# Performance work log

Measured on AMD Instinct MI355X. Metric: run time of the kernel, lower is better.

The kernel has to match this reference:

```python
import jax, jax.numpy as jnp
import numpy as np

B, T, K = 8, 512, 8
V_WORD, V_BIWORD, V_GAZ = 100000, 200000, 300000
D_WORD, D_BIWORD, D_GAZ = 50, 50, 50
HIDDEN = 256
H = HIDDEN // 2          # per-direction lattice LSTM hidden
D_IN = D_WORD + D_BIWORD # use_bigram=True
N_LABELS = 20


def setup_inputs() -> dict:
    key = jax.random.key(0)
    ks = jax.random.split(key, 16)
    word_inputs = jax.random.randint(ks[0], (B, T), 0, V_WORD)
    biword_inputs = jax.random.randint(ks[1], (B, T), 0, V_BIWORD)
    gaz_word_ids = jax.random.randint(ks[2], (B, T, K), 0, V_GAZ)
    lengths = jax.random.randint(ks[3], (B, T, K), 2, 10)  # lexicon word length in [2,9]
    pos = jnp.arange(T)[None, :, None]
    starts = pos - lengths + 1  # state index of the word's start position
    present = jax.random.bernoulli(ks[4], 0.4, (B, T, K))
    gaz_mask = present & (starts >= 0)
    gaz_starts = jnp.clip(starts, 0)
    mask = jnp.ones((B, T), dtype=jnp.int32)

    def u(k, shape, fan):
        s = 1.0 / np.sqrt(fan)
        return jax.random.uniform(k, shape, jnp.float32, -s, s)

    return dict(
        word_inputs=word_inputs, biword_inputs=biword_inputs,
        gaz_word_ids=gaz_word_ids, gaz_starts=gaz_starts,
        gaz_mask=gaz_mask, mask=mask,
        word_table=u(ks[5], (V_WORD, D_WORD), D_WORD),
        biword_table=u(ks[6], (V_BIWORD, D_BIWORD), D_BIWORD),
        gaz_table=u(ks[7], (V_GAZ, D_GAZ), D_GAZ),
        W_ih=u(ks[8], (3 * H, D_IN), D_IN),
        W_hh=u(ks[9], (3 * H, H), H),
        b_lstm=jnp.zeros((3 * H,), jnp.float32),
        Wa_ih=u(ks[10], (H, D_IN), D_IN),
        Wa_hh=u(ks[11], (H, H), H),
        b_alpha=jnp.zeros((H,), jnp.float32),
        Ww_ih=u(ks[12], (3 * H, D_GAZ), D_GAZ),
        Ww_hh=u(ks[13], (3 * H, H), H),
        b_word=jnp.zeros((3 * H,), jnp.float32),
        W_tag=u(ks[14], (N_LABELS, HIDDEN), HIDDEN),
        b_tag=jnp.zeros((N_LABELS,), jnp.float32),
    )


def lattice_lstm(x, gaz_emb, gaz_starts, gaz_mask,
                 W_ih, W_hh, b_lstm, Wa_ih, Wa_hh, b_alpha, Ww_ih, Ww_hh, b_word):
    Bn, Tn, _ = x.shape
    Hh = W_hh.shape[1]
    h0 = jnp.zeros((Bn, Hh), x.dtype)
    c0 = jnp.zeros((Bn, Hh), x.dtype)
    hist0 = jnp.zeros((Bn, Tn, Hh), x.dtype)
    xs = (jnp.arange(Tn), x.transpose(1, 0, 2), gaz_emb.transpose(1, 0, 2, 3),
          gaz_starts.transpose(1, 0, 2), gaz_mask.transpose(1, 0, 2))

    def step(carry, inp):
        h_prev, c_prev, h_hist, c_hist = carry
        j, x_j, ge_j, s_j, m_j = inp
        # gather (h, c) at the word start positions  [B,K,H]
        h_s = jnp.take_along_axis(h_hist, s_j[..., None], axis=1)
        c_s = jnp.take_along_axis(c_hist, s_j[..., None], axis=1)
        # WordLSTMCell: word memory cells for edges ending at j
        wg = (jnp.einsum('bkd,gd->bkg', ge_j, Ww_ih)
              + jnp.einsum('bkh,gh->bkg', h_s, Ww_hh) + b_word)
        i_w, f_w, g_w = jnp.split(wg, 3, axis=-1)
        c_w = jax.nn.sigmoid(f_w) * c_s + jax.nn.sigmoid(i_w) * jnp.tanh(g_w)
        # MultiInputLSTMCell char gates (i, o, g)
        g3 = x_j @ W_ih.T + h_prev @ W_hh.T + b_lstm
        i, o, g = jnp.split(g3, 3, axis=-1)
        i, o, g = jax.nn.sigmoid(i), jax.nn.sigmoid(o), jnp.tanh(g)
        # gated aggregation over word cells: alpha = exp(sigmoid(.)), softmax with exp(i)
        alpha = jax.nn.sigmoid((x_j @ Wa_ih.T)[:, None, :]
                               + jnp.einsum('bkh,gh->bkg', c_w, Wa_hh) + b_alpha)
        mk = m_j[..., None].astype(x_j.dtype)  # [B,K,1]
        w_word = mk * jnp.exp(alpha)
        w_char = jnp.exp(i)
        c_soft = (w_char * g + (w_word * c_w).sum(1)) / (w_char + w_word.sum(1))
        c_cpl = (1.0 - i) * c_prev + i * g  # coupled path when no word edges
        has_word = m_j.any(axis=1)[:, None]
        c_new = jnp.where(has_word, c_soft, c_cpl)
        h_new = o * jnp.tanh(c_new)
        return (h_new, c_new, h_hist.at[:, j].set(h_new), c_hist.at[:, j].set(c_new)), h_new

    _, hs = jax.lax.scan(step, (h0, c0, hist0, hist0), xs)
    return hs.transpose(1, 0, 2)  # [B,T,H]


def reference(word_inputs, biword_inputs, gaz_word_ids, gaz_starts, gaz_mask, mask,
              word_table, biword_table, gaz_table, W_ih, W_hh, b_lstm,
              Wa_ih, Wa_hh, b_alpha, Ww_ih, Ww_hh, b_word, W_tag, b_tag):
    # embedding + bigram concat (dropout is identity in eval)
    x = jnp.concatenate([word_table[word_inputs], biword_table[biword_inputs]], axis=-1)
    gaz_emb = gaz_table[gaz_word_ids]  # [B,T,K,Dg]
    fwd = lattice_lstm(x, gaz_emb, gaz_starts, gaz_mask,
                       W_ih, W_hh, b_lstm, Wa_ih, Wa_hh, b_alpha, Ww_ih, Ww_hh, b_word)
    # source bug: the 'backward' pass also calls self.forward_lstm -> identical output
    lstm_out = jnp.concatenate([fwd, fwd], axis=-1)  # [B,T,HIDDEN]
    outs = lstm_out @ W_tag.T + b_tag  # [B,T,L]
    tag_seq = jnp.argmax(outs, axis=-1)
    return mask.astype(tag_seq.dtype) * tag_seq
```

## Files before the change

### kernel.cpp

```cpp
#include <hip/hip_runtime.h>
#include <hip/hip_bf16.h>

#define BB 8
#define TT 512
#define KK 8
#define HH 128
#define G3 384
#define DIN 100
#define DG 50
#define NL 20

#if __has_builtin(__builtin_amdgcn_rcpf)
#define RCP_(x) __builtin_amdgcn_rcpf(x)
#else
#define RCP_(x) (1.0f/(x))
#endif

__device__ __forceinline__ float fexp_(float x) { return __expf(x); }
__device__ __forceinline__ float fsig_(float x) { return RCP_(1.0f + __expf(-x)); }
__device__ __forceinline__ float ftanh_(float x) {
    float e = __expf(2.0f * x);
    return 1.0f - 2.0f * RCP_(e + 1.0f);
}
__device__ __forceinline__ void barrier_() {
    asm volatile("s_waitcnt lgkmcnt(0)\n\ts_barrier" ::: "memory");
}

__global__ __launch_bounds__(512, 1)
void embed_gates_kernel(const int* __restrict__ wid, const int* __restrict__ bwid,
                        const float* __restrict__ wtab, const float* __restrict__ bwtab,
                        const float* __restrict__ Wih, const float* __restrict__ Waih,
                        const float* __restrict__ bl, const float* __restrict__ ba,
                        float* __restrict__ g3x, float* __restrict__ axo,
                        int c0, int CH)
{
    __shared__ float xs[8][104];
    const int tid = threadIdx.x;
    const int bpg = CH >> 3;
    const int b = blockIdx.x / bpg;
    const int tg = blockIdx.x % bpg;
    const int t0 = c0 + tg * 8;

    for (int idx = tid; idx < 800; idx += 512) {
        int tt = idx / 100;
        int c = idx - tt * 100;
        int t = t0 + tt;
        float v;
        if (c < 50) v = wtab[(long)wid[b * TT + t] * 50 + c];
        else        v = bwtab[(long)bwid[b * TT + t] * 50 + (c - 50)];
        xs[tt][c] = v;
    }
    __syncthreads();

    const int row = tid;
    float w[100];
    const float* wr;
    float bias;
    if (row < G3) { wr = Wih + (long)row * DIN; bias = bl[row]; }
    else          { wr = Waih + (long)(row - G3) * DIN; bias = ba[row - G3]; }
    const float4* wr4 = (const float4*)wr;
#pragma unroll
    for (int q = 0; q < 25; ++q) {
        float4 v = wr4[q];
        w[4*q] = v.x; w[4*q+1] = v.y; w[4*q+2] = v.z; w[4*q+3] = v.w;
    }
#pragma unroll 1
    for (int tt = 0; tt < 8; ++tt) {
        float a = bias;
#pragma unroll
        for (int c = 0; c < 100; ++c) a += w[c] * xs[tt][c];
        int lt = t0 - c0 + tt;
        if (row < G3) g3x[((long)b * CH + lt) * G3 + row] = a;
        else          axo[((long)b * CH + lt) * HH + (row - G3)] = a;
    }
}

__global__ __launch_bounds__(384, 1)
void gaz_gates_kernel(const int* __restrict__ gids, const float* __restrict__ gtab,
                      const float* __restrict__ Wwih, const float* __restrict__ bw,
                      float* __restrict__ gwT, int c0, int CH)
{
    __shared__ float ges[64][52];
    const int tid = threadIdx.x;
    const int bpg = CH >> 3;
    const int b = blockIdx.x / bpg;
    const int tg = blockIdx.x % bpg;
    const int t0 = c0 + tg * 8;

    for (int idx = tid; idx < 64 * 50; idx += 384) {
        int p = idx / 50;
        int c = idx - p * 50;
        int tt = p >> 3, k = p & 7;
        int gid = gids[((long)(b * TT + t0 + tt)) * KK + k];
        ges[p][c] = gtab[(long)gid * DG + c];
    }
    __syncthreads();

    const int row = tid;
    float w[50];
    const float2* wr2 = (const float2*)(Wwih + (long)row * DG);
#pragma unroll
    for (int q = 0; q < 25; ++q) { float2 v = wr2[q]; w[2*q] = v.x; w[2*q+1] = v.y; }
    const float bias = bw[row];
    const int lt0 = t0 - c0;
#pragma unroll 1
    for (int p = 0; p < 64; ++p) {
        float a = bias;
#pragma unroll
        for (int c = 0; c < 50; ++c) a += w[c] * ges[p][c];
        int tt = p >> 3, k = p & 7;
        gwT[((long)(b * CH + lt0 + tt) * KK + k) * G3 + row] = a;
    }
}

__global__ __attribute__((amdgpu_flat_work_group_size(512, 512), amdgpu_waves_per_eu(2, 2)))
void lattice_scan_kernel(const float* __restrict__ g3x, const float* __restrict__ axb,
                         const float* __restrict__ gwT, const int* __restrict__ gstarts,
                         const int* __restrict__ gmask,
                         const float* __restrict__ Whh, const float* __restrict__ Wwhh,
                         const float* __restrict__ Wahh,
                         float* __restrict__ hs, float* __restrict__ state,
                         int c0, int CH)
{
    __shared__ float cring[8][132];
    __shared__ float cwS[8][132];
    __shared__ float wwh[8][388];
    __shared__ float whh[G3];
    __shared__ float hcur[HH];
    __shared__ float vmkF[8];
    __shared__ float WwL[256 * 128];

    const int t = threadIdx.x;
    const int b = blockIdx.x;
    const int lane = t & 63;
    const int kB = t >> 6;
    const int rq = t >> 2, q4 = t & 3;
    const int rr = t >> 1, hE = t & 1;

    float W0[HH], WAr[32];
    {
        const float4* rp = (t < G3) ? (const float4*)(Whh + (long)t * HH)
                                    : (const float4*)(Wwhh + (long)(t - G3) * HH);
#pragma unroll
        for (int q = 0; q < 32; ++q) {
            float4 v = rp[q];
            W0[4*q] = v.x; W0[4*q+1] = v.y; W0[4*q+2] = v.z; W0[4*q+3] = v.w;
        }
#pragma unroll
        for (int i = 0; i < 8; ++i) {
            float4 v = *(const float4*)(Wahh + (long)rq * HH + 16 * i + 4 * q4);
            WAr[4*i]=v.x; WAr[4*i+1]=v.y; WAr[4*i+2]=v.z; WAr[4*i+3]=v.w;
        }
    }
    for (int idx = t; idx < 256 * 128; idx += 512) {
        int r = idx >> 7, c = idx & 127;
        int cblk = c >> 2;
        int sb = cblk ^ (r & 7) ^ ((cblk >> 4) << 2);
        WwL[r * 128 + (sb << 2) + (c & 3)] = Wwhh[(long)(128 + r) * HH + c];
    }

    float* st = state + (long)b * 4480;
    if (c0 == 0) {
        for (int idx = t; idx < 8 * 132; idx += 512) ((float*)cring)[idx] = 0.f;
        for (int idx = t; idx < 8 * 388; idx += 512) ((float*)wwh)[idx] = 0.f;
        for (int idx = t; idx < G3; idx += 512) whh[idx] = 0.f;
    } else {
        for (int idx = t; idx < 1024; idx += 512) cring[idx >> 7][idx & 127] = st[idx];
        for (int idx = t; idx < 3072; idx += 512) wwh[idx / 384][idx % 384] = st[1024 + idx];
        for (int idx = t; idx < 384; idx += 512) whh[idx] = st[4096 + idx];
    }
    barrier_();

    const long gwstep = (long)KK * G3;
    const float* gwB = gwT + (long)b * CH * gwstep + (long)kB * G3 + 2 * lane;
    const long g3base = (long)b * CH * G3;
    const long axbase = (long)b * CH * HH;

    float2 pA = *(const float2*)(gwB);
    float2 pF = *(const float2*)(gwB + 128);
    float2 pG = *(const float2*)(gwB + 256);
    int rs = gstarts[(b * TT + c0) * KK + kB];
    int rm = gmask  [(b * TT + c0) * KK + kB];
    float pg0 = g3x[g3base + rq];
    float pg1 = g3x[g3base + rq + 128];
    float pg2 = g3x[g3base + rq + 256];
    float pax = axb[axbase + rq];

    for (int j = c0; j < c0 + CH; ++j) {
        const int lt = j - c0;
        const int slot = rs & 7;
        const bool valid = (rm != 0);
        const float2 cA = pA, cF = pF, cG = pG;
        const float dg0 = pg0, dg1 = pg1, dg2 = pg2, dax = pax;

        if (lane == 0) vmkF[kB] = valid ? 1.0f : 0.0f;

        if (lt + 1 < CH) {
            const float* gw = gwB + (long)(lt + 1) * gwstep;
            pA = *(const float2*)(gw);
            pF = *(const float2*)(gw + 128);
            pG = *(const float2*)(gw + 256);
            rs = gstarts[(b * TT + j + 1) * KK + kB];
            rm = gmask  [(b * TT + j + 1) * KK + kB];
            pg0 = g3x[g3base + (long)(lt + 1) * G3 + rq];
            pg1 = g3x[g3base + (long)(lt + 1) * G3 + rq + 128];
            pg2 = g3x[g3base + (long)(lt + 1) * G3 + rq + 256];
            pax = axb[axbase + (long)(lt + 1) * HH + rq];
        }

        {
            const int r2 = 2 * lane;
            float2 wi = *(const float2*)&wwh[slot][r2];
            float2 wf = *(const float2*)&wwh[slot][r2 + 128];
            float2 wg = *(const float2*)&wwh[slot][r2 + 256];
            float2 cs = *(const float2*)&cring[slot][r2];
            float2 cw;
            cw.x = fsig_(cF.x + wf.x) * cs.x + fsig_(cA.x + wi.x) * ftanh_(cG.x + wg.x);
            cw.y = fsig_(cF.y + wf.y) * cs.y + fsig_(cA.y + wi.y) * ftanh_(cG.y + wg.y);
            *(float2*)&cwS[kB][r2] = cw;
        }
        barrier_();

        const float4 vk0 = *(const float4*)&vmkF[0];
        const float4 vk1 = *(const float4*)&vmkF[4];
        const float vmk[8] = {vk0.x, vk0.y, vk0.z, vk0.w, vk1.x, vk1.y, vk1.z, vk1.w};
        const bool hw_any = (vk0.x + vk0.y + vk0.z + vk0.w + vk1.x + vk1.y + vk1.z + vk1.w) > 0.f;

        float sumw = 0.f, sumwc = 0.f;
#pragma unroll
        for (int k = 0; k < 8; ++k) {
            if (vmk[k] != 0.f) {
                float a0 = 0.f, a1 = 0.f;
#pragma unroll
                for (int i = 0; i < 8; i += 2) {
                    float4 c0v = *(const float4*)&cwS[k][16 * i + 4 * q4];
                    float4 c1v = *(const float4*)&cwS[k][16 * (i + 1) + 4 * q4];
                    a0 += WAr[4*i]*c0v.x + WAr[4*i+1]*c0v.y + WAr[4*i+2]*c0v.z + WAr[4*i+3]*c0v.w;
                    a1 += WAr[4*i+4]*c1v.x + WAr[4*i+5]*c1v.y + WAr[4*i+6]*c1v.z + WAr[4*i+7]*c1v.w;
                }
                float acc = a0 + a1;
                acc += __shfl_xor(acc, 1);
                acc += __shfl_xor(acc, 2);
                float al = fsig_(dax + acc);
                float w = fexp_(al);
                sumw += w;
                sumwc += w * cwS[k][rq];
            }
        }

        float i_ = fsig_(dg0 + whh[rq]);
        float o_ = fsig_(dg1 + whh[rq + 128]);
        float g_ = ftanh_(dg2 + whh[rq + 256]);
        float cprev = cring[(j - 1) & 7][rq];
        float wc = fexp_(i_);
        float csoft = (wc * g_ + sumwc) / (wc + sumw);
        float ccpl = (1.f - i_) * cprev + i_ * g_;
        float cn = hw_any ? csoft : ccpl;
        float hn = o_ * ftanh_(cn);
        if (q4 == 0) {
            cring[j & 7][rq] = cn;
            hcur[rq] = hn;
            hs[((long)b * CH + lt) * HH + rq] = hn;
        }
        barrier_();

        {
            const float4* h4 = (const float4*)hcur;
            float a0 = 0.f, a1 = 0.f, a2 = 0.f, a3 = 0.f;
#pragma unroll
            for (int q = 0; q < 8; ++q) {
                float4 h0 = h4[4*q], h1 = h4[4*q+1], h2 = h4[4*q+2], h3 = h4[4*q+3];
                a0 += W0[16*q+0]*h0.x + W0[16*q+1]*h0.y + W0[16*q+2]*h0.z + W0[16*q+3]*h0.w;
                a1 += W0[16*q+4]*h1.x + W0[16*q+5]*h1.y + W0[16*q+6]*h1.z + W0[16*q+7]*h1.w;
                a2 += W0[16*q+8]*h2.x + W0[16*q+9]*h2.y + W0[16*q+10]*h2.z + W0[16*q+11]*h2.w;
                a3 += W0[16*q+12]*h3.x + W0[16*q+13]*h3.y + W0[16*q+14]*h3.z + W0[16*q+15]*h3.w;
            }
            float e0 = (a0 + a1) + (a2 + a3);
            if (t < G3) whh[t] = e0;
            else        wwh[j & 7][t - G3] = e0;
        }
        {
            const float4* h4 = (const float4*)hcur;
            float s0 = 0.f, s1 = 0.f;
#pragma unroll
            for (int cb = 0; cb < 16; cb += 2) {
                int cblk0 = cb | (hE << 4);
                int cblk1 = (cb + 1) | (hE << 4);
                int sb0 = cblk0 ^ (rr & 7) ^ (hE << 2);
                int sb1 = cblk1 ^ (rr & 7) ^ (hE << 2);
                float4 w0 = *(const float4*)&WwL[rr * 128 + (sb0 << 2)];
                float4 w1 = *(const float4*)&WwL[rr * 128 + (sb1 << 2)];
                float4 h0 = h4[cblk0], h1 = h4[cblk1];
                s0 += w0.x*h0.x + w0.y*h0.y + w0.z*h0.z + w0.w*h0.w;
                s1 += w1.x*h1.x + w1.y*h1.y + w1.z*h1.z + w1.w*h1.w;
            }
            float s = s0 + s1;
            s += __shfl_xor(s, 1);
            if (hE == 0) wwh[j & 7][128 + rr] = s;
        }
        barrier_();
    }

    for (int idx = t; idx < 1024; idx += 512) st[idx] = cring[idx >> 7][idx & 127];
    for (int idx = t; idx < 3072; idx += 512) st[1024 + idx] = wwh[idx / 384][idx % 384];
    for (int idx = t; idx < 384; idx += 512) st[4096 + idx] = whh[idx];
}

__global__ __launch_bounds__(320, 1)
void tag_kernel(const float* __restrict__ hs, const float* __restrict__ Wtag,
                const float* __restrict__ btag, const int* __restrict__ maskp,
                int* __restrict__ out, int c0, int CH)
{
    __shared__ float ht[16][132];
    __shared__ float lg[16][20];
    const int tid = threadIdx.x;
    const int bpg = CH >> 4;
    const int b = blockIdx.x / bpg;
    const int tg = blockIdx.x % bpg;
    const int lt0 = tg * 16;

    for (int idx = tid; idx < 16 * 128; idx += 320)
        ht[idx >> 7][idx & 127] = hs[((long)b * CH + lt0 + (idx >> 7)) * HH + (idx & 127)];
    __syncthreads();

    {
        int tl = tid / 20, l = tid - tl * 20;
        float a = btag[l];
        const float* w0 = Wtag + (long)l * 256;
#pragma unroll
        for (int r = 0; r < 128; ++r) a += (w0[r] + w0[r + 128]) * ht[tl][r];
        lg[tl][l] = a;
    }
    __syncthreads();
    if (tid < 16) {
        float best = lg[tid][0];
        int bi = 0;
#pragma unroll
        for (int l = 1; l < NL; ++l) {
            float v = lg[tid][l];
            if (v > best) { best = v; bi = l; }
        }
        int t = c0 + lt0 + tid;
        out[b * TT + t] = maskp[b * TT + t] * bi;
    }
}

extern "C" void kernel_launch(void* const* d_in, const int* in_sizes, int n_in,
                              void* d_out, int out_size, void* d_ws, size_t ws_size,
                              hipStream_t stream) {
    const int* word_inputs   = (const int*)d_in[0];
    const int* biword_inputs = (const int*)d_in[1];
    const int* gaz_word_ids  = (const int*)d_in[2];
    const int* gaz_starts    = (const int*)d_in[3];
    const int* gaz_mask      = (const int*)d_in[4];
    const int* maskp         = (const int*)d_in[5];
    const float* word_table   = (const float*)d_in[6];
    const float* biword_table = (const float*)d_in[7];
    const float* gaz_table    = (const float*)d_in[8];
    const float* W_ih   = (const float*)d_in[9];
    const float* W_hh   = (const float*)d_in[10];
    const float* b_lstm = (const float*)d_in[11];
    const float* Wa_ih  = (const float*)d_in[12];
    const float* Wa_hh  = (const float*)d_in[13];
    const float* b_alpha= (const float*)d_in[14];
    const float* Ww_ih  = (const float*)d_in[15];
    const float* Ww_hh  = (const float*)d_in[16];
    const float* b_word = (const float*)d_in[17];
    const float* W_tag  = (const float*)d_in[18];
    const float* b_tag  = (const float*)d_in[19];
    int* out = (int*)d_out;
    float* ws = (float*)d_ws;

    int CH = 16;
    if      (ws_size >= 118784UL * 512 + 143360UL) CH = 512;
    else if (ws_size >= 118784UL * 128 + 143360UL) CH = 128;
    else if (ws_size >= 118784UL *  32 + 143360UL) CH = 32;

    float* g3x = ws;
    float* axb = g3x + 8L * CH * 384;
    float* gwT = axb + 8L * CH * 128;
    float* hsb = gwT + 8L * CH * 3072;
    float* stb = hsb + 8L * CH * 128;

    for (int c0 = 0; c0 < TT; c0 += CH) {
        embed_gates_kernel<<<CH, 512, 0, stream>>>(word_inputs, biword_inputs,
                                                   word_table, biword_table,
                                                   W_ih, Wa_ih, b_lstm, b_alpha,
                                                   g3x, axb, c0, CH);
        gaz_gates_kernel<<<CH, 384, 0, stream>>>(gaz_word_ids, gaz_table,
                                                 Ww_ih, b_word, gwT, c0, CH);
        lattice_scan_kernel<<<BB, 512, 0, stream>>>(g3x, axb, gwT, gaz_starts, gaz_mask,
                                                    W_hh, Ww_hh, Wa_hh, hsb, stb, c0, CH);
        tag_kernel<<<CH / 2, 320, 0, stream>>>(hsb, W_tag, b_tag, maskp, out, c0, CH);
    }
}
```

Measured before the change: 1.968 ms.

## Stream recurrent weight rows from global memory per step instead of register-resident

Drops the 128-float per-thread register copy of the W_hh/Ww_hh row. Each step now re-reads the row from global/L2 in staged chunks (12, 16 and 4 float4s), issued ahead of their use so the loads overlap other work. The next-step prefetch of gate inputs is also moved later in the step. This lowers register pressure and likely spills, at the cost of per-step global reads of 256 KB of weights on the serial recurrence path.

```diff
diff --git a/kernel.cpp b/kernel.cpp
--- a/kernel.cpp
+++ b/kernel.cpp
@@ -137,20 +137,11 @@
     const int rq = t >> 2, q4 = t & 3;
     const int rr = t >> 1, hE = t & 1;
 
-    float W0[HH], WAr[32];
-    {
-        const float4* rp = (t < G3) ? (const float4*)(Whh + (long)t * HH)
-                                    : (const float4*)(Wwhh + (long)(t - G3) * HH);
-#pragma unroll
-        for (int q = 0; q < 32; ++q) {
-            float4 v = rp[q];
-            W0[4*q] = v.x; W0[4*q+1] = v.y; W0[4*q+2] = v.z; W0[4*q+3] = v.w;
-        }
-#pragma unroll
-        for (int i = 0; i < 8; ++i) {
-            float4 v = *(const float4*)(Wahh + (long)rq * HH + 16 * i + 4 * q4);
-            WAr[4*i]=v.x; WAr[4*i+1]=v.y; WAr[4*i+2]=v.z; WAr[4*i+3]=v.w;
-        }
+    float WAr[32];
+#pragma unroll
+    for (int i = 0; i < 8; ++i) {
+        float4 v = *(const float4*)(Wahh + (long)rq * HH + 16 * i + 4 * q4);
+        WAr[4*i]=v.x; WAr[4*i+1]=v.y; WAr[4*i+2]=v.z; WAr[4*i+3]=v.w;
     }
     for (int idx = t; idx < 256 * 128; idx += 512) {
         int r = idx >> 7, c = idx & 127;
@@ -158,6 +149,8 @@
         int sb = cblk ^ (r & 7) ^ ((cblk >> 4) << 2);
         WwL[r * 128 + (sb << 2) + (c & 3)] = Wwhh[(long)(128 + r) * HH + c];
     }
+    const float4* wrow4 = (t < G3) ? (const float4*)(Whh + (long)t * HH)
+                                   : (const float4*)(Wwhh + (long)(t - G3) * HH);
 
     float* st = state + (long)b * 4480;
     if (c0 == 0) {
@@ -195,18 +188,9 @@
 
         if (lane == 0) vmkF[kB] = valid ? 1.0f : 0.0f;
 
-        if (lt + 1 < CH) {
-            const float* gw = gwB + (long)(lt + 1) * gwstep;
-            pA = *(const float2*)(gw);
-            pF = *(const float2*)(gw + 128);
-            pG = *(const float2*)(gw + 256);
-            rs = gstarts[(b * TT + j + 1) * KK + kB];
-            rm = gmask  [(b * TT + j + 1) * KK + kB];
-            pg0 = g3x[g3base + (long)(lt + 1) * G3 + rq];
-            pg1 = g3x[g3base + (long)(lt + 1) * G3 + rq + 128];
-            pg2 = g3x[g3base + (long)(lt + 1) * G3 + rq + 256];
-            pax = axb[axbase + (long)(lt + 1) * HH + rq];
-        }
+        float4 wbufA[12];
+#pragma unroll
+        for (int i = 0; i < 12; ++i) wbufA[i] = wrow4[i];
 
         {
             const int r2 = 2 * lane;
@@ -248,6 +232,19 @@
             }
         }
 
+        if (lt + 1 < CH) {
+            const float* gw = gwB + (long)(lt + 1) * gwstep;
+            pA = *(const float2*)(gw);
+            pF = *(const float2*)(gw + 128);
+            pG = *(const float2*)(gw + 256);
+            rs = gstarts[(b * TT + j + 1) * KK + kB];
+            rm = gmask  [(b * TT + j + 1) * KK + kB];
+            pg0 = g3x[g3base + (long)(lt + 1) * G3 + rq];
+            pg1 = g3x[g3base + (long)(lt + 1) * G3 + rq + 128];
+            pg2 = g3x[g3base + (long)(lt + 1) * G3 + rq + 256];
+            pax = axb[axbase + (long)(lt + 1) * HH + rq];
+        }
+
         float i_ = fsig_(dg0 + whh[rq]);
         float o_ = fsig_(dg1 + whh[rq + 128]);
         float g_ = ftanh_(dg2 + whh[rq + 256]);
@@ -264,23 +261,19 @@
         }
         barrier_();
 
+        const float4* h4 = (const float4*)hcur;
+        float a0 = 0.f, a1 = 0.f, a2 = 0.f, a3 = 0.f;
+#pragma unroll
+        for (int i = 0; i < 12; ++i) {
+            float4 w = wbufA[i], h = h4[i];
+            a0 = fmaf(w.x, h.x, a0); a1 = fmaf(w.y, h.y, a1);
+            a2 = fmaf(w.z, h.z, a2); a3 = fmaf(w.w, h.w, a3);
+        }
+        float4 wbufB[16];
+#pragma unroll
+        for (int i = 0; i < 16; ++i) wbufB[i] = wrow4[12 + i];
+
         {
-            const float4* h4 = (const float4*)hcur;
-            float a0 = 0.f, a1 = 0.f, a2 = 0.f, a3 = 0.f;
-#pragma unroll
-            for (int q = 0; q < 8; ++q) {
-                float4 h0 = h4[4*q], h1 = h4[4*q+1], h2 = h4[4*q+2], h3 = h4[4*q+3];
-                a0 += W0[16*q+0]*h0.x + W0[16*q+1]*h0.y + W0[16*q+2]*h0.z + W0[16*q+3]*h0.w;
-                a1 += W0[16*q+4]*h1.x + W0[16*q+5]*h1.y + W0[16*q+6]*h1.z + W0[16*q+7]*h1.w;
-                a2 += W0[16*q+8]*h2.x + W0[16*q+9]*h2.y + W0[16*q+10]*h2.z + W0[16*q+11]*h2.w;
-                a3 += W0[16*q+12]*h3.x + W0[16*q+13]*h3.y + W0[16*q+14]*h3.z + W0[16*q+15]*h3.w;
-            }
-            float e0 = (a0 + a1) + (a2 + a3);
-            if (t < G3) whh[t] = e0;
-            else        wwh[j & 7][t - G3] = e0;
-        }
-        {
-            const float4* h4 = (const float4*)hcur;
             float s0 = 0.f, s1 = 0.f;
 #pragma unroll
             for (int cb = 0; cb < 16; cb += 2) {
@@ -297,6 +290,24 @@
             float s = s0 + s1;
             s += __shfl_xor(s, 1);
             if (hE == 0) wwh[j & 7][128 + rr] = s;
+        }
+
+        {
+#pragma unroll
+            for (int i = 0; i < 16; ++i) {
+                float4 w = wbufB[i], h = h4[12 + i];
+                a0 = fmaf(w.x, h.x, a0); a1 = fmaf(w.y, h.y, a1);
+                a2 = fmaf(w.z, h.z, a2); a3 = fmaf(w.w, h.w, a3);
+            }
+#pragma unroll
+            for (int i = 0; i < 4; ++i) {
+                float4 w = wrow4[28 + i], h = h4[28 + i];
+                a0 = fmaf(w.x, h.x, a0); a1 = fmaf(w.y, h.y, a1);
+                a2 = fmaf(w.z, h.z, a2); a3 = fmaf(w.w, h.w, a3);
+            }
+            float e0 = (a0 + a1) + (a2 + a3);
+            if (t < G3) whh[t] = e0;
+            else        wwh[j & 7][t - G3] = e0;
         }
         barrier_();
     }
```

Measured after the change: 4.281 ms. 118% more time.

## Stream W_hh from global per step and split Ww_hh rows across quad lanes

Applied to the files above, without the earlier changes.

The 128-float per-thread register copy of the W_hh/Ww_hh row is removed. The first 128 rows of Ww_hh are now computed by four-lane groups, each holding 8 float4 in registers and combining results with shuffles. The W_hh matvec for the 384 gate rows reads weights from global memory (L1/L2) on every timestep. This cuts register pressure and the spilling it caused, but adds a global load on the serial recurrence critical path and leaves the W_hh work to only 384 of 512 threads.

```diff
diff --git a/kernel.cpp b/kernel.cpp
--- a/kernel.cpp
+++ b/kernel.cpp
@@ -137,27 +137,24 @@
     const int rq = t >> 2, q4 = t & 3;
     const int rr = t >> 1, hE = t & 1;
 
-    float W0[HH], WAr[32];
-    {
-        const float4* rp = (t < G3) ? (const float4*)(Whh + (long)t * HH)
-                                    : (const float4*)(Wwhh + (long)(t - G3) * HH);
-#pragma unroll
-        for (int q = 0; q < 32; ++q) {
-            float4 v = rp[q];
-            W0[4*q] = v.x; W0[4*q+1] = v.y; W0[4*q+2] = v.z; W0[4*q+3] = v.w;
-        }
-#pragma unroll
-        for (int i = 0; i < 8; ++i) {
-            float4 v = *(const float4*)(Wahh + (long)rq * HH + 16 * i + 4 * q4);
-            WAr[4*i]=v.x; WAr[4*i+1]=v.y; WAr[4*i+2]=v.z; WAr[4*i+3]=v.w;
-        }
-    }
+    float WAr[32];
+#pragma unroll
+    for (int i = 0; i < 8; ++i) {
+        float4 v = *(const float4*)(Wahh + (long)rq * HH + 16 * i + 4 * q4);
+        WAr[4*i]=v.x; WAr[4*i+1]=v.y; WAr[4*i+2]=v.z; WAr[4*i+3]=v.w;
+    }
+    float4 Wq[8];
+#pragma unroll
+    for (int m = 0; m < 8; ++m)
+        Wq[m] = *(const float4*)(Wwhh + (long)rq * HH + (4 * m + q4) * 4);
+
     for (int idx = t; idx < 256 * 128; idx += 512) {
         int r = idx >> 7, c = idx & 127;
         int cblk = c >> 2;
         int sb = cblk ^ (r & 7) ^ ((cblk >> 4) << 2);
         WwL[r * 128 + (sb << 2) + (c & 3)] = Wwhh[(long)(128 + r) * HH + c];
     }
+    const float4* wrow4 = (const float4*)(Whh + (long)(t < G3 ? t : 0) * HH);
 
     float* st = state + (long)b * 4480;
     if (c0 == 0) {
@@ -264,23 +261,40 @@
         }
         barrier_();
 
+        const float4* h4 = (const float4*)hcur;
+
         {
-            const float4* h4 = (const float4*)hcur;
             float a0 = 0.f, a1 = 0.f, a2 = 0.f, a3 = 0.f;
 #pragma unroll
+            for (int m = 0; m < 8; ++m) {
+                float4 w = Wq[m];
+                float4 h = h4[4 * m + q4];
+                a0 = fmaf(w.x, h.x, a0); a1 = fmaf(w.y, h.y, a1);
+                a2 = fmaf(w.z, h.z, a2); a3 = fmaf(w.w, h.w, a3);
+            }
+            float e = (a0 + a1) + (a2 + a3);
+            e += __shfl_xor(e, 1);
+            e += __shfl_xor(e, 2);
+            if (q4 == 0) wwh[j & 7][rq] = e;
+        }
+
+        if (t < G3) {
+            float a0 = 0.f, a1 = 0.f, a2 = 0.f, a3 = 0.f;
+#pragma unroll
             for (int q = 0; q < 8; ++q) {
-                float4 h0 = h4[4*q], h1 = h4[4*q+1], h2 = h4[4*q+2], h3 = h4[4*q+3];
-                a0 += W0[16*q+0]*h0.x + W0[16*q+1]*h0.y + W0[16*q+2]*h0.z + W0[16*q+3]*h0.w;
-                a1 += W0[16*q+4]*h1.x + W0[16*q+5]*h1.y + W0[16*q+6]*h1.z + W0[16*q+7]*h1.w;
-                a2 += W0[16*q+8]*h2.x + W0[16*q+9]*h2.y + W0[16*q+10]*h2.z + W0[16*q+11]*h2.w;
-                a3 += W0[16*q+12]*h3.x + W0[16*q+13]*h3.y + W0[16*q+14]*h3.z + W0[16*q+15]*h3.w;
+                float4 w0 = wrow4[4*q],   h0 = h4[4*q];
+                float4 w1 = wrow4[4*q+1], h1 = h4[4*q+1];
+                float4 w2 = wrow4[4*q+2], h2 = h4[4*q+2];
+                float4 w3 = wrow4[4*q+3], h3 = h4[4*q+3];
+                a0 += w0.x*h0.x + w0.y*h0.y + w0.z*h0.z + w0.w*h0.w;
+                a1 += w1.x*h1.x + w1.y*h1.y + w1.z*h1.z + w1.w*h1.w;
+                a2 += w2.x*h2.x + w2.y*h2.y + w2.z*h2.z + w2.w*h2.w;
+                a3 += w3.x*h3.x + w3.y*h3.y + w3.z*h3.z + w3.w*h3.w;
             }
-            float e0 = (a0 + a1) + (a2 + a3);
-            if (t < G3) whh[t] = e0;
-            else        wwh[j & 7][t - G3] = e0;
-        }
+            whh[t] = (a0 + a1) + (a2 + a3);
+        }
+
         {
-            const float4* h4 = (const float4*)hcur;
             float s0 = 0.f, s1 = 0.f;
 #pragma unroll
             for (int cb = 0; cb < 16; cb += 2) {
```

Result: slower. 4.281 ms (+117.5%).
